# Kernel tuning notes

Measured on AMD Instinct MI355X. Metric: run time of the kernel, lower is better.

The kernel has to match this reference:

```python
import jax, jax.numpy as jnp
import numpy as np

H = 49      # hidden_size
L = 7       # num_layers
I = 7       # input_size
O = 7       # output_size
B, T = 1024, 512


def setup_inputs() -> dict:
    key = jax.random.key(0)
    ks = jax.random.split(key, 8)
    s = 1.0 / np.sqrt(H).astype(np.float32)  # torch LSTM init scale
    x = jax.random.normal(ks[0], (B, T, I), dtype=jnp.float32)
    # PyTorch gate order: i, f, g, o stacked along first dim of W (4H rows).
    W_ih0 = jax.random.normal(ks[1], (4 * H, I), dtype=jnp.float32) * s      # layer 0 input weights
    W_ih_rest = jax.random.normal(ks[2], (L - 1, 4 * H, H), dtype=jnp.float32) * s  # layers 1..6
    W_hh = jax.random.normal(ks[3], (L, 4 * H, H), dtype=jnp.float32) * s
    b_ih = jax.random.normal(ks[4], (L, 4 * H), dtype=jnp.float32) * s
    b_hh = jax.random.normal(ks[5], (L, 4 * H), dtype=jnp.float32) * s
    fc_w = jax.random.normal(ks[6], (O, H), dtype=jnp.float32) * s
    fc_b = jax.random.normal(ks[7], (O,), dtype=jnp.float32) * s
    return dict(x=x, W_ih0=W_ih0, W_ih_rest=W_ih_rest, W_hh=W_hh,
                b_ih=b_ih, b_hh=b_hh, fc_w=fc_w, fc_b=fc_b)


def _lstm_layer(xs, Wih, Whh, bias):
    """One LSTM layer. xs: [B, T, Din] -> [B, T, H]. Zero initial (h, c)."""
    Bq = xs.shape[0]
    # Precompute input-to-gate projections for all timesteps: [T, B, 4H]
    pre = jnp.einsum('btd,gd->tbg', xs, Wih) + bias

    def step(carry, p_t):
        h, c = carry
        gates = p_t + h @ Whh.T                      # [B, 4H]
        i, f, g, o = jnp.split(gates, 4, axis=-1)    # torch order i,f,g,o
        i = jax.nn.sigmoid(i)
        f = jax.nn.sigmoid(f)
        g = jnp.tanh(g)
        o = jax.nn.sigmoid(o)
        c = f * c + i * g
        h = o * jnp.tanh(c)
        return (h, c), h

    h0 = jnp.zeros((Bq, H), xs.dtype)
    c0 = jnp.zeros((Bq, H), xs.dtype)
    _, hs = jax.lax.scan(step, (h0, c0), pre)        # hs: [T, B, H]
    return hs.transpose(1, 0, 2)


def reference(x, W_ih0, W_ih_rest, W_hh, b_ih, b_hh, fc_w, fc_b):
    h = _lstm_layer(x, W_ih0, W_hh[0], b_ih[0] + b_hh[0])
    for l in range(1, L):
        h = _lstm_layer(h, W_ih_rest[l - 1], W_hh[l], b_ih[l] + b_hh[l])
    return h @ fc_w.T + fc_b                         # [B, T, O]
```

## Files before the change

kernel.cpp:

```cpp
#include <hip/hip_runtime.h>
#include <math.h>


constexpr int TT = 512;
constexpr int BB = 1024;
constexpr int HH = 49;
constexpr int GG = 196;

constexpr int RW = 16;
constexpr int SLOT_STEP = 832;
constexpr int SLOT_BLK  = 8 * SLOT_STEP;
constexpr size_t R_GRP       = (size_t)RW * SLOT_BLK;
constexpr size_t R_LAYER     = 64ull * R_GRP;
constexpr size_t RING_FLOATS = 3ull * R_LAYER;
constexpr size_t FLAG_INTS   = 6ull * 64 * 32;
constexpr size_t WS_NEEDED   = RING_FLOATS * 4 + FLAG_INTS * 4;

typedef __attribute__((ext_vector_type(8))) short short8;
typedef __attribute__((ext_vector_type(4))) short short4v;
typedef __attribute__((ext_vector_type(4))) float f32x4;

__device__ __forceinline__ float sigmoidf_(float x) {
    return 1.0f / (1.0f + __expf(-x));
}
__device__ __forceinline__ float tanhf_(float x) {
    return 1.0f - 2.0f / (1.0f + __expf(2.0f * x));
}

__device__ __forceinline__ void bf16split(float x, short& hi, short& lo) {
    unsigned u = __float_as_uint(x);
    unsigned r = u + 0x7FFFu + ((u >> 16) & 1u);
    hi = (short)(r >> 16);
    float fhi = __uint_as_float(r & 0xFFFF0000u);
    float rem = x - fhi;
    unsigned u2 = __float_as_uint(rem);
    unsigned r2 = u2 + 0x7FFFu + ((u2 >> 16) & 1u);
    lo = (short)(r2 >> 16);
}

__device__ __forceinline__ int addr2B(int m, int k) {
    return (k >> 5) * 512 + ((k >> 3) & 3) * 128 + m * 8 + (k & 7);
}

__device__ __forceinline__ float ring_ldf(const float* p) {
    return __hip_atomic_load(p, __ATOMIC_RELAXED, __HIP_MEMORY_SCOPE_AGENT);
}
__device__ __forceinline__ void ring_st(float* p, float v) {
    __hip_atomic_store(p, v, __ATOMIC_RELAXED, __HIP_MEMORY_SCOPE_AGENT);
}
__device__ __forceinline__ int flag_ld(const int* p) {
    return __hip_atomic_load(p, __ATOMIC_RELAXED, __HIP_MEMORY_SCOPE_AGENT);
}
__device__ __forceinline__ void flag_st(int* p, int v) {
    __hip_atomic_store(p, v, __ATOMIC_RELAXED, __HIP_MEMORY_SCOPE_AGENT);
}

#define WGBAR() asm volatile("s_waitcnt lgkmcnt(0)\n\ts_barrier" ::: "memory")
#define VMDRAIN() asm volatile("s_waitcnt vmcnt(0)" ::: "memory")

__global__ void zero_flags(int* f, int n) {
    int i = blockIdx.x * 256 + threadIdx.x;
    if (i < n) f[i] = 0;
}

__global__ __launch_bounds__(896, 1)
void lstm_pair(const float* __restrict__ xin,
               float* __restrict__ ring,
               int* __restrict__ flags,
               const float* __restrict__ Wih0,
               const float* __restrict__ Wihr,
               const float* __restrict__ Whh,
               const float* __restrict__ bih,
               const float* __restrict__ bhh,
               const float* __restrict__ fcw,
               const float* __restrict__ fcb,
               float* __restrict__ outp)
{
    __shared__ __align__(16) short Ahi[2][2][2048];
    __shared__ __align__(16) short Alo[2][2][2048];
    __shared__ __align__(16) float preT[2][13 * 16 * 20];
    __shared__ __align__(16) float h_st[2][13 * 64];
    __shared__ __align__(16) float h_sh[2][16][52];
    __shared__ __align__(16) float w7[7][52];
    __shared__ float bsh[8];

    const int tid  = threadIdx.x;
    const int wave = tid >> 6;
    const int half = wave >= 7;
    const int w7i  = wave - (half ? 7 : 0);
    const int lane = tid & 63;
    const int quad = lane >> 4;
    const int lrow = lane & 15;
    const int tloc = tid - 448;

    const int cls = blockIdx.x >> 6;
    const int grp = blockIdx.x & 63;
    const int b0  = grp << 4;

    const int  lay   = half ? (2 * cls + 1) : (2 * cls);
    const bool laok  = !half || (cls < 3);
    const int  layc  = laok ? lay : 0;
    const int  DIN   = (layc == 0) ? 7 : 49;
    const int  KSRT  = (layc == 0) ? 2 : 4;
    const float* Wih = (layc == 0) ? Wih0 : (Wihr + (size_t)(layc - 1) * GG * HH);
    const float* Whl = Whh + (size_t)layc * GG * HH;
    const float* bi  = bih + (size_t)layc * GG;
    const float* bh  = bhh + (size_t)layc * GG;

    const int rc_out = cls;
    const int rc_in  = cls - 1;
    float* rout_g = ring + (size_t)(cls < 3 ? rc_out : 0) * R_LAYER
                         + (size_t)grp * R_GRP;
    const float* rin_g = ring + (size_t)(cls > 0 ? rc_in : 0) * R_LAYER
                              + (size_t)grp * R_GRP;
    int* flag_out  = flags + (size_t)((cls < 3 ? rc_out : 0) * 64 + grp) * 32;
    int* cons_poll = flags + (size_t)((3 + (cls < 3 ? rc_out : 0)) * 64 + grp) * 32;
    int* flag_in   = flags + (size_t)((cls > 0 ? rc_in : 0) * 64 + grp) * 32;
    int* cons_sig  = flags + (size_t)((3 + (cls > 0 ? rc_in : 0)) * 64 + grp) * 32;

    const int ntiles = (w7i < 6) ? 2 : 1;
    const int tA = (w7i < 6) ? w7i : 12;
    const int tB = w7i + 6;

    short8 BH[2][4], BL[2][4];
    float  biasv[2];
    #pragma unroll
    for (int ti = 0; ti < 2; ++ti) {
        const int  nt    = ti ? tB : tA;
        const bool valid = laok && (ti < ntiles) && (nt < 13);
        const int  np    = nt * 16 + lrow;
        const int  j     = np >> 2;
        const int  g     = np & 3;
        const bool jb    = valid && (j < HH);
        biasv[ti] = jb ? (bi[g * HH + j] + bh[g * HH + j]) : 0.0f;
        #pragma unroll
        for (int ks = 0; ks < 4; ++ks) {
            #pragma unroll
            for (int jj = 0; jj < 8; ++jj) {
                const int k = ks * 32 + quad * 8 + jj;
                float wv = 0.0f;
                if (jb) {
                    const int r = g * HH + j;
                    if (k < HH)                       wv = Whl[r * HH + k];
                    else if (k >= 52 && k < 52 + DIN) wv = Wih[r * DIN + (k - 52)];
                }
                short h_, l_;
                bf16split(wv, h_, l_);
                BH[ti][ks][jj] = h_;
                BL[ti][ks][jj] = l_;
            }
        }
    }

    const int  j0 = 4 * tA + quad;
    const int  j1 = 4 * tB + quad;
    const bool v1 = (w7i < 6);
    const int  ah0 = addr2B(lrow, j0);
    const int  ah1 = addr2B(lrow, j1);
    const int  bx0 = addr2B(lrow, 52 + j0);
    const int  bx1 = addr2B(lrow, 52 + j1);
    float cc0 = 0.0f, cc1 = 0.0f;

    const bool is_stw = half && (cls < 3) && (w7i >= 4);
    const int  st_t0  = (w7i - 4) * 4;
    const int  st_ntt = (w7i == 6) ? 5 : 4;

    bool is_ld = false;
    int  a_st = 0;
    const float* gb = xin;
    if (!half) {
        if (cls == 0) {
            is_ld = (tid < 112);
            const int m  = tid / 7;
            const int kx = tid - m * 7;
            a_st = addr2B(m & 15, 52 + kx);
            gb   = xin + ((size_t)(b0 + (m & 15)) * TT) * 7 + kx;
        } else {
            is_ld = (tid < 208);
            const int jc   = tid >> 4;
            const int samp = tid & 15;
            a_st = addr2B(samp, 52 + 4 * jc);
            gb   = rin_g + (size_t)(4 * jc) * 16 + samp;
        }
    }

    for (int i = tid; i < 4096; i += 896) {
        ((unsigned*)Ahi)[i] = 0u;
        ((unsigned*)Alo)[i] = 0u;
    }
    if (cls == 3) {
        for (int i = tid; i < 2 * 16 * 52; i += 896) ((float*)h_sh)[i] = 0.0f;
        for (int i = tid; i < 7 * 52; i += 896) {
            const int o = i / 52, k = i - o * 52;
            w7[o][k] = (k < HH) ? fcw[o * HH + k] : 0.0f;
        }
        if (tid < 7) bsh[tid] = fcb[tid];
    }
    __syncthreads();

    if (cls > 0) {
        if (tid == 208) {
            while (flag_ld(flag_in) < 1) __builtin_amdgcn_s_sleep(1);
        }
        WGBAR();
    }

    float4 xO = {0, 0, 0, 0}, xE = {0, 0, 0, 0};
    if (is_ld) {
        if (cls == 0) {
            short h_, l_;
            bf16split(gb[0], h_, l_);
            Ahi[0][0][a_st] = h_; Alo[0][0][a_st] = l_;
            xO.x = gb[7];
        } else {
            float4 x0;
            x0.x = ring_ldf(gb);      x0.y = ring_ldf(gb + 16);
            x0.z = ring_ldf(gb + 32); x0.w = ring_ldf(gb + 48);
            xO.x = ring_ldf(gb + SLOT_STEP);      xO.y = ring_ldf(gb + SLOT_STEP + 16);
            xO.z = ring_ldf(gb + SLOT_STEP + 32); xO.w = ring_ldf(gb + SLOT_STEP + 48);
            short h0,l0_,h1,l1_,h2,l2_,h3,l3_;
            bf16split(x0.x,h0,l0_); bf16split(x0.y,h1,l1_);
            bf16split(x0.z,h2,l2_); bf16split(x0.w,h3,l3_);
            short4v vh = {h0,h1,h2,h3}, vl = {l0_,l1_,l2_,l3_};
            *(short4v*)&Ahi[0][0][a_st] = vh;
            *(short4v*)&Alo[0][0][a_st] = vl;
        }
    }
    __syncthreads();

    auto body = [&](int i, float4& xUse, float4& xFill) {
        const int pa  = i & 1;
        const int tba = i & 7;
        const int t_b = i - 1;
        const int tbb = t_b & 7;
        const int p2  = t_b & 1;
        const bool aAct = (i < TT);
        const bool bAct = half && (cls < 3) && (i >= 1);

        if (bAct) {
            if (tbb == 2) VMDRAIN();
            if (tbb == 3 && (t_b >> 3) >= 1 && tid == 704)
                flag_st(flag_out, t_b >> 3);
            if (is_stw && i >= 2) {
                const int tp   = t_b - 1;
                const int offp = ((tp >> 3) & (RW - 1)) * SLOT_BLK
                               + (tp & 7) * SLOT_STEP;
                const float* hs = h_st[p2 ^ 1];
                #pragma unroll
                for (int q = 0; q < 5; ++q) {
                    if (q < st_ntt) {
                        const int tt = st_t0 + q;
                        ring_st(rout_g + offp + tt * 64 + lane, hs[tt * 64 + lane]);
                    }
                }
            }
        }

        if (cls > 0 && tba == 6 && (i + 2) < TT) {
            if (tid == 208) {
                const int want = ((i + 2) >> 3) + 1;
                while (flag_ld(flag_in) < want) __builtin_amdgcn_s_sleep(1);
            }
            WGBAR();
        }
        if (cls > 0 && i < TT && tba == 7 && tid == 256)
            flag_st(cons_sig, (i >> 3) + 1);

        if (!half && aAct) {
            const bool ldnow = is_ld && (i + 2) < TT;
            if (ldnow) {
                if (cls == 0) {
                    xFill.x = gb[(size_t)(i + 2) * 7];
                } else {
                    const int offn = (((i + 2) >> 3) & (RW - 1)) * SLOT_BLK
                                   + ((i + 2) & 7) * SLOT_STEP;
                    xFill.x = ring_ldf(gb + offn);
                    xFill.y = ring_ldf(gb + offn + 16);
                    xFill.z = ring_ldf(gb + offn + 32);
                    xFill.w = ring_ldf(gb + offn + 48);
                }
            }

            short8 AH[4], AL[4];
            #pragma unroll
            for (int ks = 0; ks < 4; ++ks) {
                if (ks < KSRT) {
                    AH[ks] = *(const short8*)&Ahi[0][pa][ks * 512 + lane * 8];
                    AL[ks] = *(const short8*)&Alo[0][pa][ks * 512 + lane * 8];
                }
            }
            f32x4 C0 = {biasv[0], biasv[0], biasv[0], biasv[0]};
            #pragma unroll
            for (int ks = 0; ks < 4; ++ks) {
                if (ks < KSRT) {
                    C0 = __builtin_amdgcn_mfma_f32_16x16x32_bf16(AH[ks], BH[0][ks], C0, 0, 0, 0);
                    C0 = __builtin_amdgcn_mfma_f32_16x16x32_bf16(AL[ks], BH[0][ks], C0, 0, 0, 0);
                    C0 = __builtin_amdgcn_mfma_f32_16x16x32_bf16(AH[ks], BL[0][ks], C0, 0, 0, 0);
                }
            }
            #pragma unroll
            for (int r = 0; r < 4; ++r)
                preT[0][(tA * 16 + 4 * quad + r) * 20 + lrow] = C0[r];
            if (w7i < 6) {
                f32x4 C1 = {biasv[1], biasv[1], biasv[1], biasv[1]};
                #pragma unroll
                for (int ks = 0; ks < 4; ++ks) {
                    if (ks < KSRT) {
                        C1 = __builtin_amdgcn_mfma_f32_16x16x32_bf16(AH[ks], BH[1][ks], C1, 0, 0, 0);
                        C1 = __builtin_amdgcn_mfma_f32_16x16x32_bf16(AL[ks], BH[1][ks], C1, 0, 0, 0);
                        C1 = __builtin_amdgcn_mfma_f32_16x16x32_bf16(AH[ks], BL[1][ks], C1, 0, 0, 0);
                    }
                }
                #pragma unroll
                for (int r = 0; r < 4; ++r)
                    preT[0][(tB * 16 + 4 * quad + r) * 20 + lrow] = C1[r];
            }

            {
                const f32x4 gt = *(const f32x4*)&preT[0][(tA * 16 + lrow) * 20 + 4 * quad];
                const float i_ = sigmoidf_(gt.x);
                const float f_ = sigmoidf_(gt.y);
                const float g_ = tanhf_(gt.z);
                const float o_ = sigmoidf_(gt.w);
                cc0 = f_ * cc0 + i_ * g_;
                const float hv = o_ * tanhf_(cc0);
                short hh, hl;
                bf16split(hv, hh, hl);
                Ahi[0][pa ^ 1][ah0] = hh;
                Alo[0][pa ^ 1][ah0] = hl;
                if (cls < 3) {
                    Ahi[1][pa ^ 1][bx0] = hh;
                    Alo[1][pa ^ 1][bx0] = hl;
                } else {
                    h_sh[pa ^ 1][lrow][j0] = hv;
                }
            }
            if (v1) {
                const f32x4 gt = *(const f32x4*)&preT[0][(tB * 16 + lrow) * 20 + 4 * quad];
                const float i_ = sigmoidf_(gt.x);
                const float f_ = sigmoidf_(gt.y);
                const float g_ = tanhf_(gt.z);
                const float o_ = sigmoidf_(gt.w);
                cc1 = f_ * cc1 + i_ * g_;
                const float hv = o_ * tanhf_(cc1);
                short hh, hl;
                bf16split(hv, hh, hl);
                Ahi[0][pa ^ 1][ah1] = hh;
                Alo[0][pa ^ 1][ah1] = hl;
                if (cls < 3) {
                    Ahi[1][pa ^ 1][bx1] = hh;
                    Alo[1][pa ^ 1][bx1] = hl;
                } else {
                    h_sh[pa ^ 1][lrow][j1] = hv;
                }
            }

            if (is_ld && (i + 1) < TT) {
                if (cls == 0) {
                    short h_, l_;
                    bf16split(xUse.x, h_, l_);
                    Ahi[0][pa ^ 1][a_st] = h_; Alo[0][pa ^ 1][a_st] = l_;
                } else {
                    short h0,l0_,h1,l1_,h2,l2_,h3,l3_;
                    bf16split(xUse.x,h0,l0_); bf16split(xUse.y,h1,l1_);
                    bf16split(xUse.z,h2,l2_); bf16split(xUse.w,h3,l3_);
                    short4v vh = {h0,h1,h2,h3}, vl = {l0_,l1_,l2_,l3_};
                    *(short4v*)&Ahi[0][pa ^ 1][a_st] = vh;
                    *(short4v*)&Alo[0][pa ^ 1][a_st] = vl;
                }
            }
        } else if (bAct) {
            short8 AH[4], AL[4];
            #pragma unroll
            for (int ks = 0; ks < 4; ++ks) {
                AH[ks] = *(const short8*)&Ahi[1][pa][ks * 512 + lane * 8];
                AL[ks] = *(const short8*)&Alo[1][pa][ks * 512 + lane * 8];
            }
            f32x4 C0 = {biasv[0], biasv[0], biasv[0], biasv[0]};
            #pragma unroll
            for (int ks = 0; ks < 4; ++ks) {
                C0 = __builtin_amdgcn_mfma_f32_16x16x32_bf16(AH[ks], BH[0][ks], C0, 0, 0, 0);
                C0 = __builtin_amdgcn_mfma_f32_16x16x32_bf16(AL[ks], BH[0][ks], C0, 0, 0, 0);
                C0 = __builtin_amdgcn_mfma_f32_16x16x32_bf16(AH[ks], BL[0][ks], C0, 0, 0, 0);
            }
            #pragma unroll
            for (int r = 0; r < 4; ++r)
                preT[1][(tA * 16 + 4 * quad + r) * 20 + lrow] = C0[r];
            if (w7i < 6) {
                f32x4 C1 = {biasv[1], biasv[1], biasv[1], biasv[1]};
                #pragma unroll
                for (int ks = 0; ks < 4; ++ks) {
                    C1 = __builtin_amdgcn_mfma_f32_16x16x32_bf16(AH[ks], BH[1][ks], C1, 0, 0, 0);
                    C1 = __builtin_amdgcn_mfma_f32_16x16x32_bf16(AL[ks], BH[1][ks], C1, 0, 0, 0);
                    C1 = __builtin_amdgcn_mfma_f32_16x16x32_bf16(AH[ks], BL[1][ks], C1, 0, 0, 0);
                }
                #pragma unroll
                for (int r = 0; r < 4; ++r)
                    preT[1][(tB * 16 + 4 * quad + r) * 20 + lrow] = C1[r];
            }

            {
                const f32x4 gt = *(const f32x4*)&preT[1][(tA * 16 + lrow) * 20 + 4 * quad];
                const float i_ = sigmoidf_(gt.x);
                const float f_ = sigmoidf_(gt.y);
                const float g_ = tanhf_(gt.z);
                const float o_ = sigmoidf_(gt.w);
                cc0 = f_ * cc0 + i_ * g_;
                const float hv = o_ * tanhf_(cc0);
                short hh, hl;
                bf16split(hv, hh, hl);
                Ahi[1][pa ^ 1][ah0] = hh;
                Alo[1][pa ^ 1][ah0] = hl;
                h_st[p2][tA * 64 + lane] = hv;
            }
            if (v1) {
                const f32x4 gt = *(const f32x4*)&preT[1][(tB * 16 + lrow) * 20 + 4 * quad];
                const float i_ = sigmoidf_(gt.x);
                const float f_ = sigmoidf_(gt.y);
                const float g_ = tanhf_(gt.z);
                const float o_ = sigmoidf_(gt.w);
                cc1 = f_ * cc1 + i_ * g_;
                const float hv = o_ * tanhf_(cc1);
                short hh, hl;
                bf16split(hv, hh, hl);
                Ahi[1][pa ^ 1][ah1] = hh;
                Alo[1][pa ^ 1][ah1] = hl;
                h_st[p2][tB * 64 + lane] = hv;
            }
        }

        if (cls == 3 && half && tloc < 112 && i >= 1) {
            const int s = tloc / 7;
            const int o = tloc - s * 7;
            const float* hr = h_sh[pa][s];
            float acc = bsh[o];
            #pragma unroll
            for (int k = 0; k < 52; k += 4) {
                const f32x4 hv4 = *(const f32x4*)&hr[k];
                const f32x4 wv4 = *(const f32x4*)&w7[o][k];
                acc = fmaf(hv4.x, wv4.x, acc);
                acc = fmaf(hv4.y, wv4.y, acc);
                acc = fmaf(hv4.z, wv4.z, acc);
                acc = fmaf(hv4.w, wv4.w, acc);
            }
            outp[((size_t)(b0 + s) * TT + (i - 1)) * 7 + o] = acc;
        }

        if (cls < 3 && (i & 7) == 0 && i >= RW * 8 && i < TT && tid == 208) {
            const int need = (i >> 3) - RW + 1;
            while (flag_ld(cons_poll) < need) __builtin_amdgcn_s_sleep(1);
        }

        WGBAR();
    };

    for (int ii = 0; ii < TT; ii += 2) {
        body(ii,     xO, xE);
        body(ii + 1, xE, xO);
    }
    body(TT, xO, xE);

    if (is_stw) {
        const int offp = ((511 >> 3) & (RW - 1)) * SLOT_BLK + (511 & 7) * SLOT_STEP;
        const float* hs = h_st[1];
        #pragma unroll
        for (int q = 0; q < 5; ++q) {
            if (q < st_ntt) {
                const int tt = st_t0 + q;
                ring_st(rout_g + offp + tt * 64 + lane, hs[tt * 64 + lane]);
            }
        }
    }
    if (cls < 3) {
        VMDRAIN();
        __syncthreads();
        if (tid == 704)
            flag_st(flag_out, 64);
    }
}


template<int DIN>
__global__ __launch_bounds__(448)
void lstm_fb(const float* xin, float* hout,
             const float* __restrict__ Wih, const float* __restrict__ Whh,
             const float* __restrict__ bihp, const float* __restrict__ bhhp)
{
    constexpr int XO = 52;
    constexpr int KTOT = XO + DIN;
    constexpr int KSTEPS = (KTOT + 31) / 32;
    __shared__ short Ahi[2][KSTEPS * 512];
    __shared__ short Alo[2][KSTEPS * 512];
    __shared__ float preT[13 * 64];

    const int tid = threadIdx.x, wave = tid >> 6, lane = tid & 63;
    const int quad = lane >> 4, lrow = lane & 15;
    const int b0 = blockIdx.x * 4;
    const int ntiles = (wave < 6) ? 2 : 1;
    const int tileA = (wave < 6) ? wave : 12;
    const int tileB = wave + 6;

    short8 BH[2][KSTEPS], BL[2][KSTEPS];
    float biasv[2];
    #pragma unroll
    for (int ti = 0; ti < 2; ++ti) {
        const int nt = ti ? tileB : tileA;
        const bool valid = (ti < ntiles);
        const int np = nt * 16 + lrow, j = np >> 2, g = np & 3;
        biasv[ti] = (valid && j < HH) ? (bihp[g*HH+j] + bhhp[g*HH+j]) : 0.0f;
        #pragma unroll
        for (int ks = 0; ks < KSTEPS; ++ks)
            #pragma unroll
            for (int jj = 0; jj < 8; ++jj) {
                const int k = ks * 32 + quad * 8 + jj;
                float wv = 0.0f;
                if (valid && j < HH) {
                    const int r = g * HH + j;
                    if (k < HH) wv = Whh[r * HH + k];
                    else if (k >= XO && k < KTOT) wv = Wih[r * DIN + (k - XO)];
                }
                short h_, l_; bf16split(wv, h_, l_);
                BH[ti][ks][jj] = h_; BL[ti][ks][jj] = l_;
            }
    }

    const int ec = lane & 15, ew_jj = ec >> 2, ew_m = ec & 3, ew_ti = lane >> 4;
    const bool is_ew = (lane < 32) && (ew_ti < ntiles);
    const int ew_nt = ew_ti ? tileB : tileA;
    const int ew_j = 4 * ew_nt + ew_jj;
    const bool ew_ok = is_ew && (ew_j < HH);
    const int pa0 = (ew_nt*16 + 4*ew_jj + 0)*4 + ew_m;
    const int pa1 = (ew_nt*16 + 4*ew_jj + 1)*4 + ew_m;
    const int pa2 = (ew_nt*16 + 4*ew_jj + 2)*4 + ew_m;
    const int pa3 = (ew_nt*16 + 4*ew_jj + 3)*4 + ew_m;
    const int ew_ah = addr2B(ew_m, ew_j);
    float cc = 0.0f;

    const int lx = tid;
    const bool is_loader = (lx < 4 * DIN);
    const int ld_m = is_loader ? (lx & 3) : 0, ld_k = is_loader ? (lx >> 2) : 0;
    const int xaddr = addr2B(ld_m, XO + ld_k);
    const size_t xbase = ((size_t)(b0 + ld_m) * TT) * DIN + ld_k;
    float* houtp = hout + ((size_t)(b0 + ew_m) * TT) * HH + (ew_ok ? ew_j : 0);

    for (int i = tid; i < KSTEPS * 512; i += 448) {
        ((unsigned*)Ahi)[i] = 0u; ((unsigned*)Alo)[i] = 0u;
    }
    __syncthreads();
    if (is_loader) {
        short h_, l_; bf16split(xin[xbase], h_, l_);
        Ahi[0][xaddr] = h_; Alo[0][xaddr] = l_;
    }
    __syncthreads();

    for (int t = 0; t < TT; ++t) {
        const int p = t & 1;
        float xnext = 0.0f;
        if (is_loader && (t + 1 < TT)) xnext = xin[xbase + (size_t)(t+1) * DIN];

        short8 AH[KSTEPS], AL[KSTEPS];
        #pragma unroll
        for (int ks = 0; ks < KSTEPS; ++ks) {
            AH[ks] = *(const short8*)&Ahi[p][ks * 512 + lane * 8];
            AL[ks] = *(const short8*)&Alo[p][ks * 512 + lane * 8];
        }
        #pragma unroll
        for (int ti = 0; ti < 2; ++ti) {
            f32x4 C = {biasv[ti], biasv[ti], biasv[ti], biasv[ti]};
            #pragma unroll
            for (int ks = 0; ks < KSTEPS; ++ks) {
                C = __builtin_amdgcn_mfma_f32_16x16x32_bf16(AH[ks], BH[ti][ks], C, 0, 0, 0);
                C = __builtin_amdgcn_mfma_f32_16x16x32_bf16(AL[ks], BH[ti][ks], C, 0, 0, 0);
                C = __builtin_amdgcn_mfma_f32_16x16x32_bf16(AH[ks], BL[ti][ks], C, 0, 0, 0);
            }
            if (ti < ntiles && lane < 16) {
                const int nt = ti ? tileB : tileA;
                *(f32x4*)&preT[(nt * 16 + lrow) * 4] = C;
            }
        }
        if (is_ew) {
            const float i_ = sigmoidf_(preT[pa0]);
            const float f_ = sigmoidf_(preT[pa1]);
            const float g_ = tanhf_(preT[pa2]);
            const float o_ = sigmoidf_(preT[pa3]);
            cc = f_ * cc + i_ * g_;
            const float hv = o_ * tanhf_(cc);
            if (ew_ok) {
                short hh, hl; bf16split(hv, hh, hl);
                Ahi[p ^ 1][ew_ah] = hh; Alo[p ^ 1][ew_ah] = hl;
                houtp[(size_t)t * HH] = hv;
            }
        }
        if (is_loader && (t + 1 < TT)) {
            short h_, l_; bf16split(xnext, h_, l_);
            Ahi[p ^ 1][xaddr] = h_; Alo[p ^ 1][xaddr] = l_;
        }
        __syncthreads();
    }
}

__global__ __launch_bounds__(256)
void fc_fb(const float* __restrict__ hbuf, const float* __restrict__ fcw,
           const float* __restrict__ fcb, float* __restrict__ outp)
{
    constexpr int HP = 52;
    __shared__ float w[7][HP];
    __shared__ float bsh[8];
    const int tid = threadIdx.x;
    for (int i = tid; i < 7 * HP; i += 256) {
        const int o = i / HP, k = i - o * HP;
        w[o][k] = (k < HH) ? fcw[o * HH + k] : 0.0f;
    }
    if (tid < 7) bsh[tid] = fcb[tid];
    __syncthreads();
    const size_t i = (size_t)blockIdx.x * 256 + tid;
    float acc[7];
    #pragma unroll
    for (int j = 0; j < 7; ++j) acc[j] = bsh[j];
    const float* hp = hbuf + i * HH;
    #pragma unroll
    for (int k = 0; k < HH; ++k) {
        const float hv = hp[k];
        #pragma unroll
        for (int j = 0; j < 7; ++j) acc[j] = fmaf(hv, w[j][k], acc[j]);
    }
    #pragma unroll
    for (int j = 0; j < 7; ++j) outp[i * 7 + j] = acc[j];
}

extern "C" void kernel_launch(void* const* d_in, const int* in_sizes, int n_in,
                              void* d_out, int out_size, void* d_ws, size_t ws_size,
                              hipStream_t stream)
{
    const float* x    = (const float*)d_in[0];
    const float* Wih0 = (const float*)d_in[1];
    const float* Wihr = (const float*)d_in[2];
    const float* Whh  = (const float*)d_in[3];
    const float* bih  = (const float*)d_in[4];
    const float* bhh  = (const float*)d_in[5];
    const float* fcw  = (const float*)d_in[6];
    const float* fcb  = (const float*)d_in[7];
    float* outp = (float*)d_out;

    if (ws_size >= WS_NEEDED) {
        float* ring  = (float*)d_ws;
        int*   flags = (int*)((char*)d_ws + RING_FLOATS * 4);
        zero_flags<<<(int)((FLAG_INTS + 255) / 256), 256, 0, stream>>>(
            flags, (int)FLAG_INTS);
        lstm_pair<<<256, 896, 0, stream>>>(x, ring, flags, Wih0, Wihr,
                                           Whh, bih, bhh, fcw, fcb, outp);
    } else {
        float* hbuf = (float*)d_ws;
        lstm_fb<7><<<BB / 4, 448, 0, stream>>>(x, hbuf, Wih0, Whh, bih, bhh);
        for (int l = 1; l < 7; ++l) {
            lstm_fb<49><<<BB / 4, 448, 0, stream>>>(
                hbuf, hbuf,
                Wihr + (size_t)(l - 1) * GG * HH,
                Whh  + (size_t)l * GG * HH,
                bih  + (size_t)l * GG,
                bhh  + (size_t)l * GG);
        }
        fc_fb<<<(BB * TT) / 256, 256, 0, stream>>>(hbuf, fcw, fcb, outp);
    }
}
```

Baseline: 1.993 ms.

## Batch ring stores per 8-step block and deepen input prefetch to four steps

Hidden-state outputs are now kept in a 16-slot shared buffer and written to the inter-layer ring as a whole 8-step block once per block, instead of one step at a time. The drain and publish-flag points move later within the block. Consumers wait one extra block ahead, and the input register prefetch depth grows from 2 to 4 steps. The polling duties also move to dedicated threads in the second half of the block. The intent is fewer per-step global store and flag stalls and more hiding of load latency. The cost is extra shared memory, more registers, and added pipeline latency between layers.

```diff
diff --git a/kernel.cpp b/kernel.cpp
--- a/kernel.cpp
+++ b/kernel.cpp
@@ -79,7 +79,7 @@
     __shared__ __align__(16) short Ahi[2][2][2048];
     __shared__ __align__(16) short Alo[2][2][2048];
     __shared__ __align__(16) float preT[2][13 * 16 * 20];
-    __shared__ __align__(16) float h_st[2][13 * 64];
+    __shared__ __align__(16) float h_sl[16][13 * 64];
     __shared__ __align__(16) float h_sh[2][16][52];
     __shared__ __align__(16) float w7[7][52];
     __shared__ float bsh[8];
@@ -92,6 +92,9 @@
     const int quad = lane >> 4;
     const int lrow = lane & 15;
     const int tloc = tid - 448;
+
+    const bool pollB1 = (tid == 640);
+    const bool pollH  = (tid == 641);
 
     const int cls = blockIdx.x >> 6;
     const int grp = blockIdx.x & 63;
@@ -199,25 +202,29 @@
     __syncthreads();
 
     if (cls > 0) {
-        if (tid == 208) {
-            while (flag_ld(flag_in) < 1) __builtin_amdgcn_s_sleep(1);
+        if (pollB1) {
+            while (flag_ld(flag_in) < 2) __builtin_amdgcn_s_sleep(1);
         }
         WGBAR();
     }
 
-    float4 xO = {0, 0, 0, 0}, xE = {0, 0, 0, 0};
+    float4 x0r = {0,0,0,0}, x1r = {0,0,0,0}, x2r = {0,0,0,0}, x3r = {0,0,0,0};
     if (is_ld) {
         if (cls == 0) {
             short h_, l_;
             bf16split(gb[0], h_, l_);
             Ahi[0][0][a_st] = h_; Alo[0][0][a_st] = l_;
-            xO.x = gb[7];
+            x1r.x = gb[7]; x2r.x = gb[14]; x3r.x = gb[21];
         } else {
             float4 x0;
             x0.x = ring_ldf(gb);      x0.y = ring_ldf(gb + 16);
             x0.z = ring_ldf(gb + 32); x0.w = ring_ldf(gb + 48);
-            xO.x = ring_ldf(gb + SLOT_STEP);      xO.y = ring_ldf(gb + SLOT_STEP + 16);
-            xO.z = ring_ldf(gb + SLOT_STEP + 32); xO.w = ring_ldf(gb + SLOT_STEP + 48);
+            #define LD4(dst, off) \
+                dst.x = ring_ldf(gb + (off));      dst.y = ring_ldf(gb + (off) + 16); \
+                dst.z = ring_ldf(gb + (off) + 32); dst.w = ring_ldf(gb + (off) + 48);
+            LD4(x1r, SLOT_STEP)
+            LD4(x2r, 2 * SLOT_STEP)
+            LD4(x3r, 3 * SLOT_STEP)
             short h0,l0_,h1,l1_,h2,l2_,h3,l3_;
             bf16split(x0.x,h0,l0_); bf16split(x0.y,h1,l1_);
             bf16split(x0.z,h2,l2_); bf16split(x0.w,h3,l3_);
@@ -233,32 +240,36 @@
         const int tba = i & 7;
         const int t_b = i - 1;
         const int tbb = t_b & 7;
-        const int p2  = t_b & 1;
         const bool aAct = (i < TT);
         const bool bAct = half && (cls < 3) && (i >= 1);
 
         if (bAct) {
-            if (tbb == 2) VMDRAIN();
-            if (tbb == 3 && (t_b >> 3) >= 1 && tid == 704)
+            if (is_stw && tbb == 0 && t_b >= 8) {
+                const int m    = (t_b >> 3) - 1;
+                const int offb = (m & (RW - 1)) * SLOT_BLK;
+                const int s0   = (m * 8) & 15;
+                #pragma unroll
+                for (int s = 0; s < 8; ++s) {
+                    const float* hs = h_sl[(s0 + s) & 15];
+                    #pragma unroll
+                    for (int q = 0; q < 5; ++q) {
+                        if (q < st_ntt) {
+                            const int tt = st_t0 + q;
+                            ring_st(rout_g + offb + s * SLOT_STEP + tt * 64 + lane,
+                                    hs[tt * 64 + lane]);
+                        }
+                    }
+                }
+            }
+            if (tbb == 5 && t_b >= 13) VMDRAIN();
+            if (tbb == 6 && (t_b >> 3) >= 1 && tid == 704)
                 flag_st(flag_out, t_b >> 3);
-            if (is_stw && i >= 2) {
-                const int tp   = t_b - 1;
-                const int offp = ((tp >> 3) & (RW - 1)) * SLOT_BLK
-                               + (tp & 7) * SLOT_STEP;
-                const float* hs = h_st[p2 ^ 1];
-                #pragma unroll
-                for (int q = 0; q < 5; ++q) {
-                    if (q < st_ntt) {
-                        const int tt = st_t0 + q;
-                        ring_st(rout_g + offp + tt * 64 + lane, hs[tt * 64 + lane]);
-                    }
-                }
-            }
         }
 
         if (cls > 0 && tba == 6 && (i + 2) < TT) {
-            if (tid == 208) {
-                const int want = ((i + 2) >> 3) + 1;
+            if (pollB1) {
+                int want = ((i + 2) >> 3) + 2;
+                if (want > 64) want = 64;
                 while (flag_ld(flag_in) < want) __builtin_amdgcn_s_sleep(1);
             }
             WGBAR();
@@ -267,13 +278,13 @@
             flag_st(cons_sig, (i >> 3) + 1);
 
         if (!half && aAct) {
-            const bool ldnow = is_ld && (i + 2) < TT;
+            const bool ldnow = is_ld && (i + 4) < TT;
             if (ldnow) {
                 if (cls == 0) {
-                    xFill.x = gb[(size_t)(i + 2) * 7];
+                    xFill.x = gb[(size_t)(i + 4) * 7];
                 } else {
-                    const int offn = (((i + 2) >> 3) & (RW - 1)) * SLOT_BLK
-                                   + ((i + 2) & 7) * SLOT_STEP;
+                    const int offn = (((i + 4) >> 3) & (RW - 1)) * SLOT_BLK
+                                   + ((i + 4) & 7) * SLOT_STEP;
                     xFill.x = ring_ldf(gb + offn);
                     xFill.y = ring_ldf(gb + offn + 16);
                     xFill.z = ring_ldf(gb + offn + 32);
@@ -411,7 +422,7 @@
                 bf16split(hv, hh, hl);
                 Ahi[1][pa ^ 1][ah0] = hh;
                 Alo[1][pa ^ 1][ah0] = hl;
-                h_st[p2][tA * 64 + lane] = hv;
+                h_sl[t_b & 15][tA * 64 + lane] = hv;
             }
             if (v1) {
                 const f32x4 gt = *(const f32x4*)&preT[1][(tB * 16 + lrow) * 20 + 4 * quad];
@@ -425,7 +436,7 @@
                 bf16split(hv, hh, hl);
                 Ahi[1][pa ^ 1][ah1] = hh;
                 Alo[1][pa ^ 1][ah1] = hl;
-                h_st[p2][tB * 64 + lane] = hv;
+                h_sl[t_b & 15][tB * 64 + lane] = hv;
             }
         }
 
@@ -446,7 +457,7 @@
             outp[((size_t)(b0 + s) * TT + (i - 1)) * 7 + o] = acc;
         }
 
-        if (cls < 3 && (i & 7) == 0 && i >= RW * 8 && i < TT && tid == 208) {
+        if (cls < 3 && (i & 7) == 0 && i >= RW * 8 && i < TT && pollH) {
             const int need = (i >> 3) - RW + 1;
             while (flag_ld(cons_poll) < need) __builtin_amdgcn_s_sleep(1);
         }
@@ -454,20 +465,26 @@
         WGBAR();
     };
 
-    for (int ii = 0; ii < TT; ii += 2) {
-        body(ii,     xO, xE);
-        body(ii + 1, xE, xO);
-    }
-    body(TT, xO, xE);
+    for (int ii = 0; ii < TT; ii += 4) {
+        body(ii,     x1r, x0r);
+        body(ii + 1, x2r, x1r);
+        body(ii + 2, x3r, x2r);
+        body(ii + 3, x0r, x3r);
+    }
+    body(TT, x1r, x0r);
 
     if (is_stw) {
-        const int offp = ((511 >> 3) & (RW - 1)) * SLOT_BLK + (511 & 7) * SLOT_STEP;
-        const float* hs = h_st[1];
+        const int offb = (63 & (RW - 1)) * SLOT_BLK;
         #pragma unroll
-        for (int q = 0; q < 5; ++q) {
-            if (q < st_ntt) {
-                const int tt = st_t0 + q;
-                ring_st(rout_g + offp + tt * 64 + lane, hs[tt * 64 + lane]);
+        for (int s = 0; s < 8; ++s) {
+            const float* hs = h_sl[(504 + s) & 15];
+            #pragma unroll
+            for (int q = 0; q < 5; ++q) {
+                if (q < st_ntt) {
+                    const int tt = st_t0 + q;
+                    ring_st(rout_g + offb + s * SLOT_STEP + tt * 64 + lane,
+                            hs[tt * 64 + lane]);
+                }
             }
         }
     }
```

After: 2.244 ms. 1.13x slower.
